# Performance work log

Measured on AMD Instinct MI355X. Metric: run time of the kernel, lower is better.

## Reference

```python
import jax, jax.numpy as jnp
import numpy as np

MIN_NORM = 1e-15
BALL_EPS = 1e-5  # projection margin for the Poincare ball


def _tanh(x):
    return jnp.tanh(jnp.clip(x, -15.0, 15.0))


def _artanh(x):
    return jnp.arctanh(jnp.clip(x, -1.0 + 1e-5, 1.0 - 1e-5))


def givens_rotations(r, x):
    # r, x: (N, d) with d even -> (N, d)
    g = r.reshape(r.shape[0], -1, 2)
    g = g / jnp.maximum(jnp.linalg.norm(g, axis=-1, keepdims=True), MIN_NORM)
    xp = x.reshape(x.shape[0], -1, 2)
    swap = jnp.concatenate([-xp[..., 1:], xp[..., :1]], axis=-1)
    return (g[..., :1] * xp + g[..., 1:] * swap).reshape(r.shape[0], -1)


def givens_reflection(r, x):
    g = r.reshape(r.shape[0], -1, 2)
    g = g / jnp.maximum(jnp.linalg.norm(g, axis=-1, keepdims=True), MIN_NORM)
    xp = x.reshape(x.shape[0], -1, 2)
    a = jnp.concatenate([xp[..., :1], -xp[..., 1:]], axis=-1)
    b = jnp.concatenate([xp[..., 1:], xp[..., :1]], axis=-1)
    return (g[..., :1] * a + g[..., 1:] * b).reshape(r.shape[0], -1)


def expmap0(u, c):
    sqrt_c = jnp.sqrt(c)
    u_norm = jnp.maximum(jnp.linalg.norm(u, axis=-1, keepdims=True), MIN_NORM)
    return _tanh(sqrt_c * u_norm) * u / (sqrt_c * u_norm)


def mobius_add(x, y, c):
    x2 = jnp.sum(x * x, -1, keepdims=True)
    y2 = jnp.sum(y * y, -1, keepdims=True)
    xy = jnp.sum(x * y, -1, keepdims=True)
    num = (1 + 2 * c * xy + c * y2) * x + (1 - c * x2) * y
    denom = 1 + 2 * c * xy + c * c * x2 * y2
    return num / jnp.maximum(denom, MIN_NORM)


def project(x, c):
    norm = jnp.maximum(jnp.linalg.norm(x, axis=-1, keepdims=True), MIN_NORM)
    maxnorm = (1.0 - BALL_EPS) / jnp.sqrt(c)
    return jnp.where(norm > maxnorm, x / norm * maxnorm, x)


def hyp_distance_multi_c_bmm(x, v, c):
    # x: (nc, cs, d) queries; v: (nc, ns, d) candidates; c: (nc, cs, 1) curvatures
    sqrt_c = jnp.sqrt(c)                                              # (nc, cs, 1)
    vnorm = jnp.linalg.norm(v, axis=-1, keepdims=True).transpose(0, 2, 1)  # (nc, 1, ns)
    xv = jnp.einsum('bcd,bnd->bcn', x, v) / vnorm                     # (nc, cs, ns)
    gamma = _tanh(sqrt_c * vnorm) / sqrt_c                            # (nc, cs, ns)
    x2 = jnp.sum(x * x, -1, keepdims=True)                            # (nc, cs, 1)
    c1 = 1 - 2 * c * gamma * xv + c * gamma ** 2
    c2 = 1 - c * x2
    num = jnp.sqrt(jnp.maximum(c1 ** 2 * x2 + c2 ** 2 * gamma ** 2 - 2 * c1 * c2 * gamma * xv, 0.0))
    denom = 1 - 2 * c * gamma * xv + c ** 2 * gamma ** 2 * x2
    dist = _artanh(sqrt_c * num / jnp.maximum(denom, MIN_NORM))
    return 2 * dist / sqrt_c                                          # (nc, cs, ns)


def setup_inputs() -> dict:
    key = jax.random.key(0)
    nc, cs, ns, d = 16, 1024, 1024, 512
    B = nc * cs
    ks = jax.random.split(key, 8)
    return {
        'head': jax.random.normal(ks[0], (B, d), jnp.float32),
        'head_bias': jax.random.normal(ks[1], (B, 1), jnp.float32),
        'rel': jax.random.normal(ks[2], (B, d), jnp.float32),
        'rel_diag': jax.random.normal(ks[3], (B, 2 * d), jnp.float32),
        'curvature': jax.random.normal(ks[4], (B, 1), jnp.float32),
        'context': jax.random.normal(ks[5], (B, d), jnp.float32),
        'scale': jnp.full((1,), 1.0 / np.sqrt(d), jnp.float32),
        'tail': jax.random.normal(ks[6], (nc * ns, d), jnp.float32),
        'tail_bias': jax.random.normal(ks[7], (nc * ns, 1), jnp.float32),
        'chunk_size': cs,
        'neg_sample_size': ns,
    }


def reference(head, head_bias, rel, rel_diag, curvature, context, scale, tail,
              tail_bias, chunk_size, neg_sample_size):
    num_chunk = head.shape[0] // chunk_size
    d = head.shape[-1]
    c = jax.nn.softplus(curvature)                                    # (B, 1)
    rot_mat, ref_mat = jnp.split(rel_diag, 2, axis=-1)
    rot_q = givens_rotations(rot_mat, head)[:, None, :]               # (B, 1, d)
    ref_q = givens_reflection(ref_mat, head)[:, None, :]              # (B, 1, d)
    cands = jnp.concatenate([ref_q, rot_q], axis=1)                   # (B, 2, d)
    att_w = jax.nn.softmax(
        jnp.sum(context[:, None, :] * cands * scale, -1, keepdims=True), axis=1)
    att_q = jnp.sum(att_w * cands, axis=1)                            # (B, d)
    lhs = expmap0(att_q, c)
    rel_h = expmap0(rel, c)
    res = project(mobius_add(lhs, rel_h, c), c)                       # (B, d)
    x = res.reshape(num_chunk, chunk_size, d)
    v = tail.reshape(num_chunk, neg_sample_size, d)
    c3 = c.reshape(num_chunk, chunk_size, 1)
    dist = hyp_distance_multi_c_bmm(x, v, c3)                         # (nc, cs, ns)
    score = (-dist ** 2
             + head_bias.reshape(num_chunk, chunk_size, 1)
             + tail_bias.reshape(num_chunk, 1, neg_sample_size))
    return score
```

## Files before the change

### kernel.cpp

```cpp
#include <hip/hip_runtime.h>
#include <math.h>

#define DEV static __device__ __forceinline__

constexpr float MIN_NORM = 1e-15f;
constexpr float BALL_EPS = 1e-5f;
constexpr int D = 512;

typedef float f32x4 __attribute__((ext_vector_type(4)));
typedef short short8v __attribute__((ext_vector_type(8)));
typedef unsigned short ushort8v __attribute__((ext_vector_type(8)));

DEV float wave_sum(float v) {
#pragma unroll
    for (int o = 32; o > 0; o >>= 1) v += __shfl_xor(v, o, 64);
    return v;
}

DEV float rcpf_(float x) { return __builtin_amdgcn_rcpf(x); }
DEV float rsqf_(float x) { return __builtin_amdgcn_rsqf(x); }

DEV float tanh_over_a_pos(float a) {
    const float e = __expf(-2.0f * a);
    return (1.0f - e) * rcpf_((1.0f + e) * fmaxf(a, 1e-20f));
}

DEV unsigned short f2bf(float f) {
    unsigned int u = __float_as_uint(f);
    u = (u + 0x7FFFu + ((u >> 16) & 1u)) >> 16;
    return (unsigned short)u;
}
DEV float bf2f(unsigned short h) { return __uint_as_float(((unsigned int)h) << 16); }

DEV void write_packed_row(unsigned short* pack, size_t nrow, int row,
                          int lane, ushort8v hi, ushort8v lo)
{
    const int kb  = lane >> 2;
    const int cch = lane & 3;
    const int rx  = row & 7;
    unsigned short* dst = pack + ((size_t)kb * nrow + row) * 64;
    *(ushort8v*)(dst + ((cch ^ rx) * 8))       = hi;
    *(ushort8v*)(dst + (((cch + 4) ^ rx) * 8)) = lo;
}

__global__ __launch_bounds__(256)
void prep_kernel(const float* __restrict__ head,
                 const float* __restrict__ rel,
                 const float* __restrict__ rel_diag,
                 const float* __restrict__ curvature,
                 const float* __restrict__ context,
                 const float* __restrict__ scale_p,
                 const float* __restrict__ tail,
                 unsigned short* __restrict__ packA,
                 unsigned short* __restrict__ packB,
                 float* __restrict__ row_x2,
                 float* __restrict__ row_c,
                 float* __restrict__ row_sc,
                 float* __restrict__ vnorm,
                 int B, int T)
{
    const int lane = threadIdx.x & 63;
    const int base = lane * 8;
    const int grow = blockIdx.x * 4 + (threadIdx.x >> 6);

    if (grow >= B) {
        const int row = grow - B;
        const size_t roff = (size_t)row * D + base;
        float v[8];
        *(float4*)&v[0] = *(const float4*)(tail + roff);
        *(float4*)&v[4] = *(const float4*)(tail + roff + 4);
        float s = 0.0f;
        ushort8v hi, lo;
#pragma unroll
        for (int e = 0; e < 8; ++e) {
            s += v[e]*v[e];
            const unsigned short hb_ = f2bf(v[e]);
            hi[e] = hb_;
            lo[e] = f2bf(v[e] - bf2f(hb_));
        }
        s = wave_sum(s);
        write_packed_row(packB, (size_t)T, row, lane, hi, lo);
        if (lane == 0) vnorm[row] = sqrtf(s);
        return;
    }

    const int row = grow;
    const size_t roff = (size_t)row * D;
    const size_t doff = (size_t)row * 2 * D;

    float hv[8], rv[8], gv[8], fv[8], cxv[8];
    *(float4*)&hv[0]  = *(const float4*)(head + roff + base);
    *(float4*)&hv[4]  = *(const float4*)(head + roff + base + 4);
    *(float4*)&rv[0]  = *(const float4*)(rel + roff + base);
    *(float4*)&rv[4]  = *(const float4*)(rel + roff + base + 4);
    *(float4*)&gv[0]  = *(const float4*)(rel_diag + doff + base);
    *(float4*)&gv[4]  = *(const float4*)(rel_diag + doff + base + 4);
    *(float4*)&fv[0]  = *(const float4*)(rel_diag + doff + D + base);
    *(float4*)&fv[4]  = *(const float4*)(rel_diag + doff + D + base + 4);
    *(float4*)&cxv[0] = *(const float4*)(context + roff + base);
    *(float4*)&cxv[4] = *(const float4*)(context + roff + base + 4);

    float rq[8], rf[8];
#pragma unroll
    for (int p = 0; p < 4; ++p) {
        const float x0 = hv[2*p], x1 = hv[2*p+1];
        float g0 = gv[2*p], g1 = gv[2*p+1];
        const float gi = rsqf_(fmaxf(g0*g0 + g1*g1, 1e-30f));
        g0 *= gi; g1 *= gi;
        rq[2*p]   = g0*x0 - g1*x1;
        rq[2*p+1] = g0*x1 + g1*x0;
        float f0 = fv[2*p], f1 = fv[2*p+1];
        const float fi = rsqf_(fmaxf(f0*f0 + f1*f1, 1e-30f));
        f0 *= fi; f1 *= fi;
        rf[2*p]   = f0*x0 + f1*x1;
        rf[2*p+1] = f1*x0 - f0*x1;
    }

    float s0=0,s1=0,s2=0,s3=0,s4=0,s5=0,s6=0,s7=0;
#pragma unroll
    for (int e = 0; e < 8; ++e) {
        s0 += cxv[e]*rf[e];   s1 += cxv[e]*rq[e];
        s2 += rv[e]*rv[e];    s3 += rf[e]*rv[e];
        s4 += rq[e]*rv[e];    s5 += rf[e]*rf[e];
        s6 += rq[e]*rq[e];    s7 += rf[e]*rq[e];
    }
    s0 = wave_sum(s0); s1 = wave_sum(s1); s2 = wave_sum(s2); s3 = wave_sum(s3);
    s4 = wave_sum(s4); s5 = wave_sum(s5); s6 = wave_sum(s6); s7 = wave_sum(s7);

    const float cu = curvature[row];
    const float c  = fmaxf(cu, 0.0f) + __logf(1.0f + __expf(-fabsf(cu)));
    const float sqc = sqrtf(c);
    const float sc  = scale_p[0];

    const float a0 = s0 * sc, a1 = s1 * sc;
    const float mx = fmaxf(a0, a1);
    const float e0 = __expf(a0 - mx), e1 = __expf(a1 - mx);
    const float w0 = e0 * rcpf_(e0 + e1);
    const float w1 = 1.0f - w0;

    const float att2    = fmaxf(w0*w0*s5 + 2.0f*w0*w1*s7 + w1*w1*s6, 0.0f);
    const float attdrel = w0*s3 + w1*s4;
    const float u_att = fmaxf(sqrtf(att2), MIN_NORM);
    const float u_rel = fmaxf(sqrtf(s2), MIN_NORM);

    const float kl = tanh_over_a_pos(sqc * u_att);
    const float kr = tanh_over_a_pos(sqc * u_rel);

    const float x2 = kl*kl*att2;
    const float y2 = kr*kr*s2;
    const float xy = kl*kr*attdrel;

    const float Am  = 1.0f + 2.0f*c*xy + c*y2;
    const float Bm  = 1.0f - c*x2;
    const float inv_den = rcpf_(fmaxf(1.0f + 2.0f*c*xy + c*c*x2*y2, MIN_NORM));

    float pre[8];
    float r2p = 0.0f;
#pragma unroll
    for (int e = 0; e < 8; ++e) {
        const float attq = w0*rf[e] + w1*rq[e];
        pre[e] = (Am*kl*attq + Bm*kr*rv[e]) * inv_den;
        r2p += pre[e]*pre[e];
    }
    r2p = wave_sum(r2p);

    const float nrm  = fmaxf(sqrtf(r2p), MIN_NORM);
    const float maxn = (1.0f - BALL_EPS) * rcpf_(sqc);
    const float psc  = (nrm > maxn) ? (maxn * rcpf_(nrm)) : 1.0f;

    ushort8v hi, lo;
#pragma unroll
    for (int e = 0; e < 8; ++e) {
        const float o = pre[e] * psc;
        const unsigned short hb_ = f2bf(o);
        hi[e] = hb_;
        lo[e] = f2bf(o - bf2f(hb_));
    }
    write_packed_row(packA, (size_t)B, row, lane, hi, lo);

    if (lane == 0) {
        row_x2[row] = r2p * psc * psc;
        row_c[row]  = c;
        row_sc[row] = sqc;
    }
}

__global__ __launch_bounds__(512, 2)
void score_kernel(const unsigned short* __restrict__ packA,
                  const unsigned short* __restrict__ packB,
                  const float* __restrict__ vnorm,
                  const float* __restrict__ row_x2,
                  const float* __restrict__ row_c,
                  const float* __restrict__ row_sc,
                  const float* __restrict__ head_bias,
                  const float* __restrict__ tail_bias,
                  float* __restrict__ out,
                  int cs, int ns, int nrowA, int nrowB)
{
    extern __shared__ __align__(16) char smem[];

    const int orig = blockIdx.x;
    const int wg = (orig & 7) * 32 + (orig >> 3);
    const int bz = wg >> 4;
    const int by = (wg >> 2) & 3;
    const int bx = wg & 3;
    const int m0 = by * 256;
    const int n0 = bx * 256;

    const int tid  = threadIdx.x;
    const int lane = tid & 63;
    const int w    = tid >> 6;
    const int wr   = w >> 2, wn = w & 3;
    const int lrow = lane & 15, lg = lane >> 4;

    f32x4 acc[8][4];
#pragma unroll
    for (int i = 0; i < 8; ++i)
#pragma unroll
        for (int j = 0; j < 4; ++j) acc[i][j] = f32x4{0.f, 0.f, 0.f, 0.f};

    const int xr = (lg ^ (lrow & 7)) * 16;
    const int baseA = (wr * 128 + lrow) * 128 + xr;
    const int baseB = 32768 + (wn * 64 + lrow) * 128 + xr;

    const int s16 = (tid & 255) * 16;
    const int shi = tid >> 8;

    const char* gA = (const char*)packA + (size_t)(bz * cs + m0) * 128;
    const char* gB = (const char*)packB + (size_t)(bz * ns + n0) * 128;
    const size_t strA = (size_t)nrowA * 128;
    const size_t strB = (size_t)nrowB * 128;

#define GLL(srcp, dstp)                                                        \
    __builtin_amdgcn_global_load_lds(                                          \
        (const __attribute__((address_space(1))) unsigned int*)(srcp),         \
        (__attribute__((address_space(3))) unsigned int*)(dstp), 16, 0, 0)

#define STAGE(dstbase, srcpanel, off0, sstr)                                   \
    do { const int o_ = (off0) + s16 + shi * (sstr);                           \
         GLL((srcpanel) + o_, (dstbase) + o_); } while (0)

#define STAGE_A0(d, s) do { STAGE(d, s, 0, 4096);     STAGE(d, s, 16384, 4096); } while (0)
#define STAGE_A1(d, s) do { STAGE(d, s, 8192, 4096);  STAGE(d, s, 24576, 4096); } while (0)
#define STAGE_B0(d, s) do { STAGE(d, s, 0, 8192);     STAGE(d, s, 16384, 8192); } while (0)
#define STAGE_B1(d, s) do { STAGE(d, s, 4096, 8192);  STAGE(d, s, 20480, 8192); } while (0)

#define RD(p, off) (*(const short8v*)((p) + (off)))
#define MFMA_(A_, B_, C_) __builtin_amdgcn_mfma_f32_16x16x32_bf16(A_, B_, C_, 0, 0, 0)

#define QUAD(MOFF, NOFF)                                                       \
    do {                                                                       \
        _Pragma("unroll") for (int mm = 0; mm < 4; ++mm)                       \
        _Pragma("unroll") for (int nn = 0; nn < 2; ++nn)                       \
            acc[(MOFF)+mm][(NOFF)+nn] = MFMA_(ah[mm], bh[(NOFF)+nn], acc[(MOFF)+mm][(NOFF)+nn]); \
        _Pragma("unroll") for (int mm = 0; mm < 4; ++mm)                       \
        _Pragma("unroll") for (int nn = 0; nn < 2; ++nn)                       \
            acc[(MOFF)+mm][(NOFF)+nn] = MFMA_(ah[mm], bl[(NOFF)+nn], acc[(MOFF)+mm][(NOFF)+nn]); \
        _Pragma("unroll") for (int mm = 0; mm < 4; ++mm)                       \
        _Pragma("unroll") for (int nn = 0; nn < 2; ++nn)                       \
            acc[(MOFF)+mm][(NOFF)+nn] = MFMA_(al[mm], bh[(NOFF)+nn], acc[(MOFF)+mm][(NOFF)+nn]); \
    } while (0)

#define BAR()   __builtin_amdgcn_s_barrier()
#define PRIO(x) __builtin_amdgcn_s_setprio(x)

    STAGE_A0(smem, gA);               STAGE_A1(smem, gA);
    STAGE_B0(smem + 32768, gB);       STAGE_B1(smem + 32768, gB);
    STAGE_A0(smem + 65536, gA + strA);
    STAGE_B0(smem + 98304, gB + strB);
    STAGE_B1(smem + 98304, gB + strB);
    asm volatile("s_waitcnt vmcnt(6)" ::: "memory");
    BAR();

    short8v ah[4], al[4], bh[4], bl[4];

#pragma unroll 1
    for (int t = 0; t < 16; ++t) {
        char* cur = smem + (t & 1) * 65536;
        char* oth = smem + ((t + 1) & 1) * 65536;
        const char* gA1 = gA + (size_t)(t + 1) * strA;
        const char* gA2 = gA + (size_t)(t + 2) * strA;
        const char* gB2 = gB + (size_t)(t + 2) * strB;

        if (t < 15) STAGE_A1(oth, gA1);
#pragma unroll
        for (int m = 0; m < 4; ++m) {
            ah[m] = RD(cur, baseA + m * 2048);
            al[m] = RD(cur, (baseA ^ 64) + m * 2048);
        }
#pragma unroll
        for (int n = 0; n < 2; ++n) {
            bh[n] = RD(cur, baseB + n * 2048);
            bl[n] = RD(cur, (baseB ^ 64) + n * 2048);
        }
        BAR(); PRIO(1); QUAD(0, 0); PRIO(0); BAR();

        if (t < 14) STAGE_A0(cur, gA2);
#pragma unroll
        for (int n = 2; n < 4; ++n) {
            bh[n] = RD(cur, baseB + n * 2048);
            bl[n] = RD(cur, (baseB ^ 64) + n * 2048);
        }
        BAR(); PRIO(1); QUAD(0, 2); PRIO(0); BAR();

        if (t < 14) STAGE_B0(cur + 32768, gB2);
#pragma unroll
        for (int m = 0; m < 4; ++m) {
            ah[m] = RD(cur, baseA + 8192 + m * 2048);
            al[m] = RD(cur, (baseA ^ 64) + 8192 + m * 2048);
        }
        BAR(); PRIO(1); QUAD(4, 2); PRIO(0); BAR();

        if (t < 14) STAGE_B1(cur + 32768, gB2);
        BAR(); PRIO(1); QUAD(4, 0); PRIO(0);

        if (t <= 13)      asm volatile("s_waitcnt vmcnt(6)" ::: "memory");
        else if (t == 14) asm volatile("s_waitcnt vmcnt(0)" ::: "memory");
        BAR();
    }

    const int nbase = n0 + wn * 64 + lrow;
    float rvn[4], vnv[4], tb[4];
#pragma unroll
    for (int j = 0; j < 4; ++j) {
        const int gn = bz * ns + nbase + j * 16;
        const float vn = vnorm[gn];
        vnv[j] = vn;
        rvn[j] = 1.0f / vn;
        tb[j]  = tail_bias[gn];
    }
#pragma unroll
    for (int i = 0; i < 8; ++i) {
#pragma unroll
        for (int q = 0; q < 4; ++q) {
            const int gm = bz * cs + m0 + wr * 128 + i * 16 + lg * 4 + q;
            const float x2  = row_x2[gm];
            const float cc  = row_c[gm];
            const float scq = row_sc[gm];
            const float hb  = head_bias[gm];
            const float rscq = 1.0f / scq;
            float* orow = out + (size_t)gm * ns + nbase;
#pragma unroll
            for (int j = 0; j < 4; ++j) {
                const float xv = acc[i][j][q] * rvn[j];
                float xx = fminf(scq * vnv[j], 15.0f);
                const float ey = __expf(2.0f * xx);
                const float g  = (1.0f - 2.0f / (ey + 1.0f)) * rscq;
                const float c1 = 1.0f - 2.0f*cc*g*xv + cc*g*g;
                const float c2 = 1.0f - cc*x2;
                const float num = sqrtf(fmaxf(c1*c1*x2 + c2*c2*g*g - 2.0f*c1*c2*g*xv, 0.0f));
                const float den = fmaxf(1.0f - 2.0f*cc*g*xv + cc*cc*g*g*x2, MIN_NORM);
                float tt = scq * num * __builtin_amdgcn_rcpf(den);
                tt = fminf(tt, 1.0f - 1e-5f);
                const float ath = 0.5f * __logf((1.0f + tt) * __builtin_amdgcn_rcpf(1.0f - tt));
                const float dist = 2.0f * rscq * ath;
                orow[j * 16] = -dist * dist + hb + tb[j];
            }
        }
    }
#undef GLL
#undef STAGE
#undef STAGE_A0
#undef STAGE_A1
#undef STAGE_B0
#undef STAGE_B1
#undef RD
#undef MFMA_
#undef QUAD
#undef BAR
#undef PRIO
}

extern "C" void kernel_launch(void* const* d_in, const int* in_sizes, int n_in,
                              void* d_out, int out_size, void* d_ws, size_t ws_size,
                              hipStream_t stream)
{
    const float* head      = (const float*)d_in[0];
    const float* head_bias = (const float*)d_in[1];
    const float* rel       = (const float*)d_in[2];
    const float* rel_diag  = (const float*)d_in[3];
    const float* curvature = (const float*)d_in[4];
    const float* context   = (const float*)d_in[5];
    const float* scale     = (const float*)d_in[6];
    const float* tail      = (const float*)d_in[7];
    const float* tail_bias = (const float*)d_in[8];

    const int B  = in_sizes[1];
    const int T  = in_sizes[8];
    const int ns = out_size / B;
    const int nc = T / ns;
    const int cs = B / nc;

    unsigned short* packA = (unsigned short*)d_ws;
    unsigned short* packB = packA + (size_t)16 * B * 64;
    float* row_x2 = (float*)(packB + (size_t)16 * T * 64);
    float* row_c  = row_x2 + B;
    float* row_sc = row_c + B;
    float* vnormb = row_sc + B;

    prep_kernel<<<(B + T) / 4, 256, 0, stream>>>(head, rel, rel_diag, curvature,
                                                 context, scale, tail, packA, packB,
                                                 row_x2, row_c, row_sc, vnormb, B, T);

    (void)hipFuncSetAttribute((const void*)score_kernel,
                              hipFuncAttributeMaxDynamicSharedMemorySize, 131072);
    const int nblk = (ns / 256) * (cs / 256) * nc;
    score_kernel<<<nblk, 512, 131072, stream>>>(packA, packB, vnormb, row_x2, row_c,
                                                row_sc, head_bias, tail_bias,
                                                (float*)d_out, cs, ns, B, T);
}
```

Measured before the change: 130.3 us.

## Simplify score pipeline to whole-tile double buffering; two rows per wave in prep

The score kernel drops its fine-grained staggered prefetch schedule, which split A/B loads into halves, prefetched two steps ahead and used s_setprio with extra barriers. It now issues the full next K-tile at the start of each iteration, runs all four MFMA quads without intermediate barriers, and waits on vmcnt(0) at the end. The prep kernel processes two rows per wave, interleaving the shuffle reductions for more ILP, and launches half as many blocks. The score change cuts barrier and priority overhead but loses a prefetch stage, so load latency may be less hidden.

New measurement: 126.6 us. 2.9% less time.

```diff
diff --git a/kernel.cpp b/kernel.cpp
--- a/kernel.cpp
+++ b/kernel.cpp
@@ -10,12 +10,6 @@
 typedef float f32x4 __attribute__((ext_vector_type(4)));
 typedef short short8v __attribute__((ext_vector_type(8)));
 typedef unsigned short ushort8v __attribute__((ext_vector_type(8)));
-
-DEV float wave_sum(float v) {
-#pragma unroll
-    for (int o = 32; o > 0; o >>= 1) v += __shfl_xor(v, o, 64);
-    return v;
-}
 
 DEV float rcpf_(float x) { return __builtin_amdgcn_rcpf(x); }
 DEV float rsqf_(float x) { return __builtin_amdgcn_rsqf(x); }
@@ -61,127 +55,165 @@
 {
     const int lane = threadIdx.x & 63;
     const int base = lane * 8;
-    const int grow = blockIdx.x * 4 + (threadIdx.x >> 6);
-
-    if (grow >= B) {
-        const int row = grow - B;
-        const size_t roff = (size_t)row * D + base;
-        float v[8];
-        *(float4*)&v[0] = *(const float4*)(tail + roff);
-        *(float4*)&v[4] = *(const float4*)(tail + roff + 4);
-        float s = 0.0f;
+    const int wid  = blockIdx.x * 4 + (threadIdx.x >> 6);
+    const int r0   = wid * 2;
+
+    if (r0 >= B) {
+        const int tr = r0 - B;
+        float v[2][8];
+#pragma unroll
+        for (int rr = 0; rr < 2; ++rr) {
+            const size_t off = (size_t)(tr + rr) * D + base;
+            *(float4*)&v[rr][0] = *(const float4*)(tail + off);
+            *(float4*)&v[rr][4] = *(const float4*)(tail + off + 4);
+        }
+        float s[2] = {0.f, 0.f};
+        ushort8v hi[2], lo[2];
+#pragma unroll
+        for (int rr = 0; rr < 2; ++rr)
+#pragma unroll
+            for (int e = 0; e < 8; ++e) {
+                s[rr] += v[rr][e] * v[rr][e];
+                const unsigned short hb_ = f2bf(v[rr][e]);
+                hi[rr][e] = hb_;
+                lo[rr][e] = f2bf(v[rr][e] - bf2f(hb_));
+            }
+#pragma unroll
+        for (int o = 32; o > 0; o >>= 1)
+#pragma unroll
+            for (int rr = 0; rr < 2; ++rr)
+                s[rr] += __shfl_xor(s[rr], o, 64);
+#pragma unroll
+        for (int rr = 0; rr < 2; ++rr) {
+            write_packed_row(packB, (size_t)T, tr + rr, lane, hi[rr], lo[rr]);
+            if (lane == 0) vnorm[tr + rr] = sqrtf(s[rr]);
+        }
+        return;
+    }
+
+    float hv[2][8], rv[2][8], gv[2][8], fv[2][8], cxv[2][8];
+#pragma unroll
+    for (int rr = 0; rr < 2; ++rr) {
+        const size_t roff = (size_t)(r0 + rr) * D + base;
+        const size_t doff = (size_t)(r0 + rr) * 2 * D + base;
+        *(float4*)&hv[rr][0]  = *(const float4*)(head + roff);
+        *(float4*)&hv[rr][4]  = *(const float4*)(head + roff + 4);
+        *(float4*)&rv[rr][0]  = *(const float4*)(rel + roff);
+        *(float4*)&rv[rr][4]  = *(const float4*)(rel + roff + 4);
+        *(float4*)&gv[rr][0]  = *(const float4*)(rel_diag + doff);
+        *(float4*)&gv[rr][4]  = *(const float4*)(rel_diag + doff + 4);
+        *(float4*)&fv[rr][0]  = *(const float4*)(rel_diag + doff + D);
+        *(float4*)&fv[rr][4]  = *(const float4*)(rel_diag + doff + D + 4);
+        *(float4*)&cxv[rr][0] = *(const float4*)(context + roff);
+        *(float4*)&cxv[rr][4] = *(const float4*)(context + roff + 4);
+    }
+
+    float rq[2][8], rf[2][8];
+#pragma unroll
+    for (int rr = 0; rr < 2; ++rr)
+#pragma unroll
+        for (int p = 0; p < 4; ++p) {
+            const float x0 = hv[rr][2*p], x1 = hv[rr][2*p+1];
+            float g0 = gv[rr][2*p], g1 = gv[rr][2*p+1];
+            const float gi = rsqf_(fmaxf(g0*g0 + g1*g1, 1e-30f));
+            g0 *= gi; g1 *= gi;
+            rq[rr][2*p]   = g0*x0 - g1*x1;
+            rq[rr][2*p+1] = g0*x1 + g1*x0;
+            float f0 = fv[rr][2*p], f1 = fv[rr][2*p+1];
+            const float fi = rsqf_(fmaxf(f0*f0 + f1*f1, 1e-30f));
+            f0 *= fi; f1 *= fi;
+            rf[rr][2*p]   = f0*x0 + f1*x1;
+            rf[rr][2*p+1] = f1*x0 - f0*x1;
+        }
+
+    float s[2][8];
+#pragma unroll
+    for (int rr = 0; rr < 2; ++rr) {
+#pragma unroll
+        for (int k = 0; k < 8; ++k) s[rr][k] = 0.f;
+#pragma unroll
+        for (int e = 0; e < 8; ++e) {
+            s[rr][0] += cxv[rr][e]*rf[rr][e];   s[rr][1] += cxv[rr][e]*rq[rr][e];
+            s[rr][2] += rv[rr][e]*rv[rr][e];    s[rr][3] += rf[rr][e]*rv[rr][e];
+            s[rr][4] += rq[rr][e]*rv[rr][e];    s[rr][5] += rf[rr][e]*rf[rr][e];
+            s[rr][6] += rq[rr][e]*rq[rr][e];    s[rr][7] += rf[rr][e]*rq[rr][e];
+        }
+    }
+#pragma unroll
+    for (int o = 32; o > 0; o >>= 1)
+#pragma unroll
+        for (int rr = 0; rr < 2; ++rr)
+#pragma unroll
+            for (int k = 0; k < 8; ++k)
+                s[rr][k] += __shfl_xor(s[rr][k], o, 64);
+
+    const float sc = scale_p[0];
+    float pre[2][8], r2p[2];
+    float cS[2], sqcS[2];
+#pragma unroll
+    for (int rr = 0; rr < 2; ++rr) {
+        const float cu = curvature[r0 + rr];
+        const float c  = fmaxf(cu, 0.0f) + __logf(1.0f + __expf(-fabsf(cu)));
+        const float sqc = sqrtf(c);
+        cS[rr] = c; sqcS[rr] = sqc;
+
+        const float a0 = s[rr][0] * sc, a1 = s[rr][1] * sc;
+        const float mx = fmaxf(a0, a1);
+        const float e0 = __expf(a0 - mx), e1 = __expf(a1 - mx);
+        const float w0 = e0 * rcpf_(e0 + e1);
+        const float w1 = 1.0f - w0;
+
+        const float att2    = fmaxf(w0*w0*s[rr][5] + 2.0f*w0*w1*s[rr][7] + w1*w1*s[rr][6], 0.0f);
+        const float attdrel = w0*s[rr][3] + w1*s[rr][4];
+        const float u_att = fmaxf(sqrtf(att2), MIN_NORM);
+        const float u_rel = fmaxf(sqrtf(s[rr][2]), MIN_NORM);
+
+        const float kl = tanh_over_a_pos(sqc * u_att);
+        const float kr = tanh_over_a_pos(sqc * u_rel);
+
+        const float x2 = kl*kl*att2;
+        const float y2 = kr*kr*s[rr][2];
+        const float xy = kl*kr*attdrel;
+
+        const float Am  = 1.0f + 2.0f*c*xy + c*y2;
+        const float Bm  = 1.0f - c*x2;
+        const float inv_den = rcpf_(fmaxf(1.0f + 2.0f*c*xy + c*c*x2*y2, MIN_NORM));
+
+        r2p[rr] = 0.f;
+#pragma unroll
+        for (int e = 0; e < 8; ++e) {
+            const float attq = w0*rf[rr][e] + w1*rq[rr][e];
+            pre[rr][e] = (Am*kl*attq + Bm*kr*rv[rr][e]) * inv_den;
+            r2p[rr] += pre[rr][e]*pre[rr][e];
+        }
+    }
+#pragma unroll
+    for (int o = 32; o > 0; o >>= 1)
+#pragma unroll
+        for (int rr = 0; rr < 2; ++rr)
+            r2p[rr] += __shfl_xor(r2p[rr], o, 64);
+
+#pragma unroll
+    for (int rr = 0; rr < 2; ++rr) {
+        const float nrm  = fmaxf(sqrtf(r2p[rr]), MIN_NORM);
+        const float maxn = (1.0f - BALL_EPS) * rcpf_(sqcS[rr]);
+        const float psc  = (nrm > maxn) ? (maxn * rcpf_(nrm)) : 1.0f;
+
         ushort8v hi, lo;
 #pragma unroll
         for (int e = 0; e < 8; ++e) {
-            s += v[e]*v[e];
-            const unsigned short hb_ = f2bf(v[e]);
+            const float o = pre[rr][e] * psc;
+            const unsigned short hb_ = f2bf(o);
             hi[e] = hb_;
-            lo[e] = f2bf(v[e] - bf2f(hb_));
-        }
-        s = wave_sum(s);
-        write_packed_row(packB, (size_t)T, row, lane, hi, lo);
-        if (lane == 0) vnorm[row] = sqrtf(s);
-        return;
-    }
-
-    const int row = grow;
-    const size_t roff = (size_t)row * D;
-    const size_t doff = (size_t)row * 2 * D;
-
-    float hv[8], rv[8], gv[8], fv[8], cxv[8];
-    *(float4*)&hv[0]  = *(const float4*)(head + roff + base);
-    *(float4*)&hv[4]  = *(const float4*)(head + roff + base + 4);
-    *(float4*)&rv[0]  = *(const float4*)(rel + roff + base);
-    *(float4*)&rv[4]  = *(const float4*)(rel + roff + base + 4);
-    *(float4*)&gv[0]  = *(const float4*)(rel_diag + doff + base);
-    *(float4*)&gv[4]  = *(const float4*)(rel_diag + doff + base + 4);
-    *(float4*)&fv[0]  = *(const float4*)(rel_diag + doff + D + base);
-    *(float4*)&fv[4]  = *(const float4*)(rel_diag + doff + D + base + 4);
-    *(float4*)&cxv[0] = *(const float4*)(context + roff + base);
-    *(float4*)&cxv[4] = *(const float4*)(context + roff + base + 4);
-
-    float rq[8], rf[8];
-#pragma unroll
-    for (int p = 0; p < 4; ++p) {
-        const float x0 = hv[2*p], x1 = hv[2*p+1];
-        float g0 = gv[2*p], g1 = gv[2*p+1];
-        const float gi = rsqf_(fmaxf(g0*g0 + g1*g1, 1e-30f));
-        g0 *= gi; g1 *= gi;
-        rq[2*p]   = g0*x0 - g1*x1;
-        rq[2*p+1] = g0*x1 + g1*x0;
-        float f0 = fv[2*p], f1 = fv[2*p+1];
-        const float fi = rsqf_(fmaxf(f0*f0 + f1*f1, 1e-30f));
-        f0 *= fi; f1 *= fi;
-        rf[2*p]   = f0*x0 + f1*x1;
-        rf[2*p+1] = f1*x0 - f0*x1;
-    }
-
-    float s0=0,s1=0,s2=0,s3=0,s4=0,s5=0,s6=0,s7=0;
-#pragma unroll
-    for (int e = 0; e < 8; ++e) {
-        s0 += cxv[e]*rf[e];   s1 += cxv[e]*rq[e];
-        s2 += rv[e]*rv[e];    s3 += rf[e]*rv[e];
-        s4 += rq[e]*rv[e];    s5 += rf[e]*rf[e];
-        s6 += rq[e]*rq[e];    s7 += rf[e]*rq[e];
-    }
-    s0 = wave_sum(s0); s1 = wave_sum(s1); s2 = wave_sum(s2); s3 = wave_sum(s3);
-    s4 = wave_sum(s4); s5 = wave_sum(s5); s6 = wave_sum(s6); s7 = wave_sum(s7);
-
-    const float cu = curvature[row];
-    const float c  = fmaxf(cu, 0.0f) + __logf(1.0f + __expf(-fabsf(cu)));
-    const float sqc = sqrtf(c);
-    const float sc  = scale_p[0];
-
-    const float a0 = s0 * sc, a1 = s1 * sc;
-    const float mx = fmaxf(a0, a1);
-    const float e0 = __expf(a0 - mx), e1 = __expf(a1 - mx);
-    const float w0 = e0 * rcpf_(e0 + e1);
-    const float w1 = 1.0f - w0;
-
-    const float att2    = fmaxf(w0*w0*s5 + 2.0f*w0*w1*s7 + w1*w1*s6, 0.0f);
-    const float attdrel = w0*s3 + w1*s4;
-    const float u_att = fmaxf(sqrtf(att2), MIN_NORM);
-    const float u_rel = fmaxf(sqrtf(s2), MIN_NORM);
-
-    const float kl = tanh_over_a_pos(sqc * u_att);
-    const float kr = tanh_over_a_pos(sqc * u_rel);
-
-    const float x2 = kl*kl*att2;
-    const float y2 = kr*kr*s2;
-    const float xy = kl*kr*attdrel;
-
-    const float Am  = 1.0f + 2.0f*c*xy + c*y2;
-    const float Bm  = 1.0f - c*x2;
-    const float inv_den = rcpf_(fmaxf(1.0f + 2.0f*c*xy + c*c*x2*y2, MIN_NORM));
-
-    float pre[8];
-    float r2p = 0.0f;
-#pragma unroll
-    for (int e = 0; e < 8; ++e) {
-        const float attq = w0*rf[e] + w1*rq[e];
-        pre[e] = (Am*kl*attq + Bm*kr*rv[e]) * inv_den;
-        r2p += pre[e]*pre[e];
-    }
-    r2p = wave_sum(r2p);
-
-    const float nrm  = fmaxf(sqrtf(r2p), MIN_NORM);
-    const float maxn = (1.0f - BALL_EPS) * rcpf_(sqc);
-    const float psc  = (nrm > maxn) ? (maxn * rcpf_(nrm)) : 1.0f;
-
-    ushort8v hi, lo;
-#pragma unroll
-    for (int e = 0; e < 8; ++e) {
-        const float o = pre[e] * psc;
-        const unsigned short hb_ = f2bf(o);
-        hi[e] = hb_;
-        lo[e] = f2bf(o - bf2f(hb_));
-    }
-    write_packed_row(packA, (size_t)B, row, lane, hi, lo);
-
-    if (lane == 0) {
-        row_x2[row] = r2p * psc * psc;
-        row_c[row]  = c;
-        row_sc[row] = sqc;
+            lo[e] = f2bf(o - bf2f(hb_));
+        }
+        write_packed_row(packA, (size_t)B, r0 + rr, lane, hi, lo);
+
+        if (lane == 0) {
+            row_x2[r0 + rr] = r2p[rr] * psc * psc;
+            row_c[r0 + rr]  = cS[rr];
+            row_sc[r0 + rr] = sqcS[rr];
+        }
     }
 }
 
@@ -240,10 +272,15 @@
     do { const int o_ = (off0) + s16 + shi * (sstr);                           \
          GLL((srcpanel) + o_, (dstbase) + o_); } while (0)
 
-#define STAGE_A0(d, s) do { STAGE(d, s, 0, 4096);     STAGE(d, s, 16384, 4096); } while (0)
-#define STAGE_A1(d, s) do { STAGE(d, s, 8192, 4096);  STAGE(d, s, 24576, 4096); } while (0)
-#define STAGE_B0(d, s) do { STAGE(d, s, 0, 8192);     STAGE(d, s, 16384, 8192); } while (0)
-#define STAGE_B1(d, s) do { STAGE(d, s, 4096, 8192);  STAGE(d, s, 20480, 8192); } while (0)
+#define STAGE_ALL(dstslot, srcA, srcB)                                         \
+    do {                                                                       \
+        STAGE(dstslot, srcA, 0, 4096);      STAGE(dstslot, srcA, 16384, 4096); \
+        STAGE(dstslot, srcA, 8192, 4096);   STAGE(dstslot, srcA, 24576, 4096); \
+        STAGE((dstslot)+32768, srcB, 0, 8192);                                 \
+        STAGE((dstslot)+32768, srcB, 16384, 8192);                             \
+        STAGE((dstslot)+32768, srcB, 4096, 8192);                              \
+        STAGE((dstslot)+32768, srcB, 20480, 8192);                             \
+    } while (0)
 
 #define RD(p, off) (*(const short8v*)((p) + (off)))
 #define MFMA_(A_, B_, C_) __builtin_amdgcn_mfma_f32_16x16x32_bf16(A_, B_, C_, 0, 0, 0)
@@ -262,14 +299,10 @@
     } while (0)
 
 #define BAR()   __builtin_amdgcn_s_barrier()
-#define PRIO(x) __builtin_amdgcn_s_setprio(x)
-
-    STAGE_A0(smem, gA);               STAGE_A1(smem, gA);
-    STAGE_B0(smem + 32768, gB);       STAGE_B1(smem + 32768, gB);
-    STAGE_A0(smem + 65536, gA + strA);
-    STAGE_B0(smem + 98304, gB + strB);
-    STAGE_B1(smem + 98304, gB + strB);
-    asm volatile("s_waitcnt vmcnt(6)" ::: "memory");
+#define VM0()   asm volatile("s_waitcnt vmcnt(0)" ::: "memory")
+
+    STAGE_ALL(smem, gA, gB);
+    VM0();
     BAR();
 
     short8v ah[4], al[4], bh[4], bl[4];
@@ -278,11 +311,10 @@
     for (int t = 0; t < 16; ++t) {
         char* cur = smem + (t & 1) * 65536;
         char* oth = smem + ((t + 1) & 1) * 65536;
-        const char* gA1 = gA + (size_t)(t + 1) * strA;
-        const char* gA2 = gA + (size_t)(t + 2) * strA;
-        const char* gB2 = gB + (size_t)(t + 2) * strB;
-
-        if (t < 15) STAGE_A1(oth, gA1);
+
+        if (t < 15)
+            STAGE_ALL(oth, gA + (size_t)(t + 1) * strA, gB + (size_t)(t + 1) * strB);
+
 #pragma unroll
         for (int m = 0; m < 4; ++m) {
             ah[m] = RD(cur, baseA + m * 2048);
@@ -293,29 +325,22 @@
             bh[n] = RD(cur, baseB + n * 2048);
             bl[n] = RD(cur, (baseB ^ 64) + n * 2048);
         }
-        BAR(); PRIO(1); QUAD(0, 0); PRIO(0); BAR();
-
-        if (t < 14) STAGE_A0(cur, gA2);
+        QUAD(0, 0);
 #pragma unroll
         for (int n = 2; n < 4; ++n) {
             bh[n] = RD(cur, baseB + n * 2048);
             bl[n] = RD(cur, (baseB ^ 64) + n * 2048);
         }
-        BAR(); PRIO(1); QUAD(0, 2); PRIO(0); BAR();
-
-        if (t < 14) STAGE_B0(cur + 32768, gB2);
+        QUAD(0, 2);
 #pragma unroll
         for (int m = 0; m < 4; ++m) {
             ah[m] = RD(cur, baseA + 8192 + m * 2048);
             al[m] = RD(cur, (baseA ^ 64) + 8192 + m * 2048);
         }
-        BAR(); PRIO(1); QUAD(4, 2); PRIO(0); BAR();
-
-        if (t < 14) STAGE_B1(cur + 32768, gB2);
-        BAR(); PRIO(1); QUAD(4, 0); PRIO(0);
-
-        if (t <= 13)      asm volatile("s_waitcnt vmcnt(6)" ::: "memory");
-        else if (t == 14) asm volatile("s_waitcnt vmcnt(0)" ::: "memory");
+        QUAD(4, 2);
+        QUAD(4, 0);
+
+        VM0();
         BAR();
     }
 
@@ -360,15 +385,12 @@
     }
 #undef GLL
 #undef STAGE
-#undef STAGE_A0
-#undef STAGE_A1
-#undef STAGE_B0
-#undef STAGE_B1
+#undef STAGE_ALL
 #undef RD
 #undef MFMA_
 #undef QUAD
 #undef BAR
-#undef PRIO
+#undef VM0
 }
 
 extern "C" void kernel_launch(void* const* d_in, const int* in_sizes, int n_in,
@@ -398,7 +420,7 @@
     float* row_sc = row_c + B;
     float* vnormb = row_sc + B;
 
-    prep_kernel<<<(B + T) / 4, 256, 0, stream>>>(head, rel, rel_diag, curvature,
+    prep_kernel<<<(B + T) / 8, 256, 0, stream>>>(head, rel, rel_diag, curvature,
                                                  context, scale, tail, packA, packB,
                                                  row_x2, row_c, row_sc, vnormb, B, T);
 
```
